# Kernel optimization log

Measured on AMD Instinct MI355X. Metric: run time of the kernel, lower is better.

The kernel has to match this reference:

```python
import jax, jax.numpy as jnp
import numpy as np

K_EXPERTS = 2  # init kwarg k_experts

def _glu_mlp(x, up_w, gate_w, down_w):
    # gated MLP: down( up(x) * GELU(gate(x)) ), exact-erf GELU matching torch nn.GELU()
    h = (x @ up_w) * jax.nn.gelu(x @ gate_w, approximate=False)
    return h @ down_w

def setup_inputs() -> dict:
    key = jax.random.key(0)
    ks = jax.random.split(key, 8)
    B, S, D, I, E = 2, 2048, 1024, 512, 8
    sc = 0.02
    return {
        "x": jax.random.normal(ks[0], (B, S, D), jnp.float32),
        "gate_w": jax.random.normal(ks[1], (E, D), jnp.float32) * sc,
        "up_w": jax.random.normal(ks[2], (E, D, I), jnp.float32) * sc,
        "gproj_w": jax.random.normal(ks[3], (E, D, I), jnp.float32) * sc,
        "down_w": jax.random.normal(ks[4], (E, I, D), jnp.float32) * sc,
        "shared_up_w": jax.random.normal(ks[5], (D, I), jnp.float32) * sc,
        "shared_gate_w": jax.random.normal(ks[6], (D, I), jnp.float32) * sc,
        "shared_down_w": jax.random.normal(ks[7], (I, D), jnp.float32) * sc,
    }

def reference(x, gate_w, up_w, gproj_w, down_w, shared_up_w, shared_gate_w, shared_down_w):
    B, S, D = x.shape
    E = gate_w.shape[0]
    xf = x.reshape(-1, D)                      # [T, D]
    T = xf.shape[0]

    # --- SigmaGate: softmax over expert logits, top-k, renormalize ---
    logits = xf @ gate_w.T                     # [T, E]
    scores = jax.nn.softmax(logits, axis=-1)
    topk_w, topk_idx = jax.lax.top_k(scores, K_EXPERTS)   # [T, k]
    topk_w = topk_w / (topk_w.sum(axis=-1, keepdims=True) + 1e-20)

    # combine weights as dense [T, E] (topk indices are distinct per token)
    combine = jnp.zeros((T, E), xf.dtype).at[jnp.arange(T)[:, None], topk_idx].add(topk_w)

    # --- experts: scan over E, accumulate weighted expert outputs ---
    def step(acc, ws):
        uw, gw, dw, ce = ws                    # ce: [T] combine weight for this expert
        y_e = _glu_mlp(xf, uw, gw, dw)         # [T, D]
        return acc + ce[:, None] * y_e, None

    y, _ = jax.lax.scan(step, jnp.zeros_like(xf), (up_w, gproj_w, down_w, combine.T))

    # --- shared expert on identity ---
    y = y + _glu_mlp(xf, shared_up_w, shared_gate_w, shared_down_w)
    return y.reshape(B, S, D)
```

## Files before the change

### kernel.cpp

```cpp
#include <hip/hip_runtime.h>
#include <hip/hip_bf16.h>
#include <math.h>

#define T_TOK 4096
#define D_DIM 1024
#define I_DIM 512
#define E_EXP 8
#define KSEL 2
#define NPAIR (T_TOK * KSEL)
#define ROUTED_CAP 10240
#define SHARED_BASE ROUTED_CAP
#define RTOT (ROUTED_CAP + T_TOK)
#define MAXTILES 56
#define GRID_G (MAXTILES * 4)
#define NTRB 3456

typedef __bf16 bf16x8 __attribute__((ext_vector_type(8)));
typedef float f32x4 __attribute__((ext_vector_type(4)));
typedef unsigned short ushort8 __attribute__((ext_vector_type(8)));

constexpr size_t SZ_XB  = (size_t)T_TOK * D_DIM * 2;
constexpr size_t SZ_UG  = (size_t)E_EXP * 2 * I_DIM * D_DIM * 2;
constexpr size_t SZ_DT  = (size_t)E_EXP * I_DIM * D_DIM * 2;
constexpr size_t SZ_SUG = (size_t)2 * I_DIM * D_DIM * 2;
constexpr size_t SZ_SDT = (size_t)I_DIM * D_DIM * 2;
constexpr size_t SZ_H   = (size_t)RTOT * I_DIM * 2;
constexpr size_t SZ_Y   = (size_t)RTOT * D_DIM * 2;

constexpr size_t OFF_XB   = 0;
constexpr size_t OFF_UG   = OFF_XB  + SZ_XB;
constexpr size_t OFF_DT   = OFF_UG  + SZ_UG;
constexpr size_t OFF_SUG  = OFF_DT  + SZ_DT;
constexpr size_t OFF_SDT  = OFF_SUG + SZ_SUG;
constexpr size_t OFF_H    = OFF_SDT + SZ_SDT;
constexpr size_t OFF_Y    = OFF_H   + SZ_H;
constexpr size_t OFF_TOPKI= OFF_Y   + SZ_Y;
constexpr size_t OFF_TOPKW= OFF_TOPKI + (size_t)NPAIR * 4;
constexpr size_t OFF_INV  = OFF_TOPKW + (size_t)NPAIR * 4;
constexpr size_t OFF_PERM = OFF_INV   + (size_t)NPAIR * 4;
constexpr size_t OFF_META = OFF_PERM  + (size_t)RTOT * 4;

__device__ __forceinline__ unsigned short f2bf(float f) {
  unsigned int u = __float_as_uint(f);
  unsigned int r = (u + 0x7FFFu + ((u >> 16) & 1u)) >> 16;
  return (unsigned short)r;
}
__device__ __forceinline__ float bf2f(unsigned short s) {
  return __uint_as_float(((unsigned int)s) << 16);
}
__device__ __forceinline__ void gload_lds16(const void* g, void* l) {
  __builtin_amdgcn_global_load_lds(
      (const __attribute__((address_space(1))) void*)g,
      (__attribute__((address_space(3))) void*)l, 16, 0, 0);
}

__global__ __launch_bounds__(256) void prep_kernel(
    const float* __restrict__ x,   const float* __restrict__ gw,
    const float* __restrict__ upw, const float* __restrict__ gpw,
    const float* __restrict__ dww, const float* __restrict__ sup,
    const float* __restrict__ sgt, const float* __restrict__ sdw,
    unsigned short* __restrict__ UG, unsigned short* __restrict__ sUG,
    unsigned short* __restrict__ Dt, unsigned short* __restrict__ sDt,
    unsigned short* __restrict__ xb,
    int* __restrict__ topk_idx, float* __restrict__ topk_w) {
  __shared__ float t[64][65];
  int bid = blockIdx.x, tid = threadIdx.x;
  if (bid < NTRB) {
    const float* in; unsigned short* out;
    int R, C, xt, yt, mode;
    if (bid < 1024)      { int e = bid >> 7, s = bid & 127;
      in = upw + (size_t)e * D_DIM * I_DIM; out = UG + (size_t)e * 2 * I_DIM * D_DIM;
      R = D_DIM; C = I_DIM; xt = s & 7; yt = s >> 3; mode = 0; }
    else if (bid < 2048) { int b = bid - 1024; int e = b >> 7, s = b & 127;
      in = gpw + (size_t)e * D_DIM * I_DIM; out = UG + (size_t)e * 2 * I_DIM * D_DIM;
      R = D_DIM; C = I_DIM; xt = s & 7; yt = s >> 3; mode = 1; }
    else if (bid < 3072) { int b = bid - 2048; int e = b >> 7, s = b & 127;
      in = dww + (size_t)e * I_DIM * D_DIM; out = Dt + (size_t)e * I_DIM * D_DIM;
      R = I_DIM; C = D_DIM; xt = s & 15; yt = s >> 4; mode = 2; }
    else if (bid < 3200) { int s = bid - 3072;
      in = sup; out = sUG; R = D_DIM; C = I_DIM; xt = s & 7; yt = s >> 3; mode = 0; }
    else if (bid < 3328) { int s = bid - 3200;
      in = sgt; out = sUG; R = D_DIM; C = I_DIM; xt = s & 7; yt = s >> 3; mode = 1; }
    else                 { int s = bid - 3328;
      in = sdw; out = sDt; R = I_DIM; C = D_DIM; xt = s & 15; yt = s >> 4; mode = 2; }
    int c0 = xt * 64, r0 = yt * 64;
    int tx = tid & 63, ty = tid >> 6;
#pragma unroll
    for (int i = 0; i < 16; ++i)
      t[ty + 4 * i][tx] = in[(size_t)(r0 + ty + 4 * i) * C + c0 + tx];
    __syncthreads();
#pragma unroll
    for (int i = 0; i < 16; ++i) {
      int c = c0 + ty + 4 * i;
      int orow = (mode == 2) ? c : (((c >> 4) << 5) + (c & 15) + (mode == 1 ? 16 : 0));
      out[(size_t)orow * R + r0 + tx] = f2bf(t[tx][ty + 4 * i]);
    }
  } else {
    int lane = tid & 63;
    int tok = (bid - NTRB) * 4 + (tid >> 6);
    const float4* xr = (const float4*)(x + (size_t)tok * D_DIM);
    float4 xv[4];
#pragma unroll
    for (int j = 0; j < 4; ++j) xv[j] = xr[lane + 64 * j];
#pragma unroll
    for (int j = 0; j < 4; ++j) {
      ushort4 o;
      o.x = f2bf(xv[j].x); o.y = f2bf(xv[j].y); o.z = f2bf(xv[j].z); o.w = f2bf(xv[j].w);
      *(ushort4*)&xb[(size_t)tok * D_DIM + (lane + 64 * j) * 4] = o;
    }
    float acc[E_EXP];
#pragma unroll
    for (int e = 0; e < E_EXP; ++e) {
      const float4* gr = (const float4*)(gw + (size_t)e * D_DIM);
      float a = 0.f;
#pragma unroll
      for (int j = 0; j < 4; ++j) {
        float4 g = gr[lane + 64 * j];
        a += xv[j].x * g.x + xv[j].y * g.y + xv[j].z * g.z + xv[j].w * g.w;
      }
      acc[e] = a;
    }
#pragma unroll
    for (int off = 32; off; off >>= 1)
#pragma unroll
      for (int e = 0; e < E_EXP; ++e) acc[e] += __shfl_xor(acc[e], off, 64);
    if (lane == 0) {
      int i0 = 0; float m0 = acc[0];
#pragma unroll
      for (int e = 1; e < E_EXP; ++e) if (acc[e] > m0) { m0 = acc[e]; i0 = e; }
      int i1 = -1; float m1 = -1e30f;
#pragma unroll
      for (int e = 0; e < E_EXP; ++e) if (e != i0 && acc[e] > m1) { m1 = acc[e]; i1 = e; }
      float e1 = __expf(m1 - m0);
      float w0 = 1.0f / (1.0f + e1);
      float w1 = e1 / (1.0f + e1);
      topk_idx[2 * tok] = i0; topk_idx[2 * tok + 1] = i1;
      topk_w[2 * tok] = w0;   topk_w[2 * tok + 1] = w1;
    }
  }
}

__global__ __launch_bounds__(1024) void route_kernel(
    const int* __restrict__ tidx, int* __restrict__ meta,
    int* __restrict__ perm, int* __restrict__ inv) {
  __shared__ int els[NPAIR];
  __shared__ int cnt_iw[128][E_EXP];
  __shared__ int base_iw[128][E_EXP];
  __shared__ int ebase[E_EXP];
  __shared__ int ecnt[E_EXP];
  int tid = threadIdx.x, lane = tid & 63, wv = tid >> 6;

  for (int it = 0; it < NPAIR / 1024; ++it) {
    int g = it * 1024 + tid;
    int e = tidx[g];
    els[g] = e;
#pragma unroll
    for (int ex = 0; ex < E_EXP; ++ex) {
      unsigned long long m = __ballot(e == ex);
      if (lane == 0) cnt_iw[it * 16 + wv][ex] = __popcll(m);
    }
  }
  __syncthreads();

  if (tid < E_EXP) {
    int s = 0;
    for (int iw = 0; iw < 128; ++iw) { base_iw[iw][tid] = s; s += cnt_iw[iw][tid]; }
    ecnt[tid] = s;
  }
  __syncthreads();

  if (tid == 0) {
    int o = 0, tc = 0;
    int2* m2 = (int2*)meta;
    for (int e = 0; e < E_EXP; ++e) {
      ebase[e] = o;
      int c = ecnt[e];
      int pt = (c + 255) >> 8;
      for (int ti = 0; ti < pt; ++ti) m2[tc++] = make_int2(e, o + ti * 256);
      o += pt * 256;
    }
    for (int ti = 0; ti < T_TOK / 256; ++ti)
      m2[tc++] = make_int2(E_EXP, SHARED_BASE + ti * 256);
    for (; tc < MAXTILES; ++tc) m2[tc] = make_int2(-1, 0);
  }
  __syncthreads();

  for (int it = 0; it < NPAIR / 1024; ++it) {
    int g = it * 1024 + tid;
    int e = els[g];
    int rank = 0;
#pragma unroll
    for (int ex = 0; ex < E_EXP; ++ex) {
      unsigned long long m = __ballot(e == ex);
      if (e == ex) rank = __popcll(m & ((1ull << lane) - 1ull));
    }
    int row = ebase[e] + base_iw[it * 16 + wv][e] + rank;
    perm[row] = g >> 1;
    inv[g] = row;
  }
  for (int p = tid; p < E_EXP * 256; p += 1024) {
    int e = p >> 8, s = p & 255;
    int c = ecnt[e];
    int padn = (((c + 255) >> 8) << 8) - c;
    if (s < padn) perm[ebase[e] + c + s] = 0;
  }
  for (int t = tid; t < T_TOK; t += 1024) perm[SHARED_BASE + t] = t;
}

__global__ __launch_bounds__(512, 2) void gemm1_kernel(
    const unsigned short* __restrict__ xb, const unsigned short* __restrict__ UG,
    const unsigned short* __restrict__ sUG, unsigned short* __restrict__ H,
    const int* __restrict__ meta, const int* __restrict__ perm) {
  int orig = blockIdx.x;
  int wg = (orig & 7) * (GRID_G / 8) + (orig >> 3);
  int mt = wg >> 2, nt = wg & 3;
  int2 m2 = ((const int2*)meta)[mt];
  int e = m2.x;
  if (e < 0) return;
  int base = m2.y;
  int n0 = nt * 256;
  const unsigned short* B = (e < E_EXP) ? UG + (size_t)e * 2 * I_DIM * D_DIM : sUG;

  __shared__ unsigned short As[2 * 256 * 64];
  __shared__ unsigned short Bs[2 * 256 * 64];

  int tid = threadIdx.x, lane = tid & 63, wv = tid >> 6;
  const unsigned short *gA[4], *gB[4];
  int dL[4];
#pragma unroll
  for (int j = 0; j < 4; ++j) {
    int c = j * 512 + tid;
    int row = c >> 3, q = c & 7, qs = q ^ (row & 7);
    int tok = perm[base + row];
    gA[j] = xb + (size_t)tok * D_DIM + qs * 8;
    gB[j] = B + (size_t)(n0 + row) * D_DIM + qs * 8;
    dL[j] = (j * 512 + wv * 64) * 8;
  }

  f32x4 acc[8][4] = {};
  int wr = (wv >> 2) * 128, wc = (wv & 3) * 64;
  int l15 = lane & 15, l4 = lane >> 4;
  int sx = l15 & 7;

#define STAGE1(buf, k0) do { \
  _Pragma("unroll") \
  for (int j = 0; j < 4; ++j) { \
    gload_lds16(gA[j] + (k0), As + (buf) * 16384 + dL[j]); \
    gload_lds16(gB[j] + (k0), Bs + (buf) * 16384 + dL[j]); \
  } } while (0)

  STAGE1(0, 0);
  const int NK = D_DIM / 64;
  for (int t = 0; t < NK; ++t) {
    int cur = t & 1;
    if (t + 1 < NK) {
      STAGE1(cur ^ 1, (t + 1) * 64);
      asm volatile("s_waitcnt vmcnt(8)" ::: "memory");
    } else {
      asm volatile("s_waitcnt vmcnt(0)" ::: "memory");
    }
    __builtin_amdgcn_s_barrier();
#pragma unroll
    for (int kh = 0; kh < 2; ++kh) {
      int kb = kh * 4 + l4;
      bf16x8 af[8], bfr[4];
#pragma unroll
      for (int i = 0; i < 8; ++i)
        af[i] = *reinterpret_cast<const bf16x8*>(&As[cur * 16384 + (wr + i * 16 + l15) * 64 + ((kb ^ sx)) * 8]);
#pragma unroll
      for (int j = 0; j < 4; ++j)
        bfr[j] = *reinterpret_cast<const bf16x8*>(&Bs[cur * 16384 + (wc + j * 16 + l15) * 64 + ((kb ^ sx)) * 8]);
      __builtin_amdgcn_s_setprio(1);
#pragma unroll
      for (int i = 0; i < 8; ++i)
#pragma unroll
        for (int j = 0; j < 4; ++j)
          acc[i][j] = __builtin_amdgcn_mfma_f32_16x16x32_bf16(af[i], bfr[j], acc[i][j], 0, 0, 0);
      __builtin_amdgcn_s_setprio(0);
    }
    asm volatile("s_waitcnt lgkmcnt(0)" ::: "memory");
    __builtin_amdgcn_s_barrier();
  }
#undef STAGE1

  const float is2 = 0.70710678118654752f;
  int cb = ((n0 + wc) >> 1);
#pragma unroll
  for (int i = 0; i < 8; ++i) {
    int row = base + wr + i * 16 + l4 * 4;
#pragma unroll
    for (int p = 0; p < 2; ++p) {
      int col = cb + p * 16 + l15;
#pragma unroll
      for (int r = 0; r < 4; ++r) {
        float u = acc[i][2 * p][r], g = acc[i][2 * p + 1][r];
        float gl = 0.5f * g * (1.0f + erff(g * is2));
        H[(size_t)(row + r) * I_DIM + col] = f2bf(u * gl);
      }
    }
  }
}

__global__ __launch_bounds__(512, 2) void gemm2_kernel(
    const unsigned short* __restrict__ H, const unsigned short* __restrict__ Dt,
    const unsigned short* __restrict__ sDt, unsigned short* __restrict__ Y,
    const int* __restrict__ meta) {
  int orig = blockIdx.x;
  int wg = (orig & 7) * (GRID_G / 8) + (orig >> 3);
  int mt = wg >> 2, nt = wg & 3;
  int2 m2 = ((const int2*)meta)[mt];
  int e = m2.x;
  if (e < 0) return;
  int base = m2.y;
  int n0 = nt * 256;
  const unsigned short* B = (e < E_EXP) ? Dt + (size_t)e * D_DIM * I_DIM : sDt;

  __shared__ unsigned short As[2 * 256 * 64];
  __shared__ unsigned short Bs[2 * 256 * 64];

  int tid = threadIdx.x, lane = tid & 63, wv = tid >> 6;
  const unsigned short *gA[4], *gB[4];
  int dL[4];
#pragma unroll
  for (int j = 0; j < 4; ++j) {
    int c = j * 512 + tid;
    int row = c >> 3, q = c & 7, qs = q ^ (row & 7);
    gA[j] = H + (size_t)(base + row) * I_DIM + qs * 8;
    gB[j] = B + (size_t)(n0 + row) * I_DIM + qs * 8;
    dL[j] = (j * 512 + wv * 64) * 8;
  }

  f32x4 acc[8][4] = {};
  int wr = (wv >> 2) * 128, wc = (wv & 3) * 64;
  int l15 = lane & 15, l4 = lane >> 4;
  int sx = l15 & 7;

#define STAGE2(buf, k0) do { \
  _Pragma("unroll") \
  for (int j = 0; j < 4; ++j) { \
    gload_lds16(gA[j] + (k0), As + (buf) * 16384 + dL[j]); \
    gload_lds16(gB[j] + (k0), Bs + (buf) * 16384 + dL[j]); \
  } } while (0)

  STAGE2(0, 0);
  const int NK = I_DIM / 64;
  for (int t = 0; t < NK; ++t) {
    int cur = t & 1;
    if (t + 1 < NK) {
      STAGE2(cur ^ 1, (t + 1) * 64);
      asm volatile("s_waitcnt vmcnt(8)" ::: "memory");
    } else {
      asm volatile("s_waitcnt vmcnt(0)" ::: "memory");
    }
    __builtin_amdgcn_s_barrier();
#pragma unroll
    for (int kh = 0; kh < 2; ++kh) {
      int kb = kh * 4 + l4;
      bf16x8 af[8], bfr[4];
#pragma unroll
      for (int i = 0; i < 8; ++i)
        af[i] = *reinterpret_cast<const bf16x8*>(&As[cur * 16384 + (wr + i * 16 + l15) * 64 + ((kb ^ sx)) * 8]);
#pragma unroll
      for (int j = 0; j < 4; ++j)
        bfr[j] = *reinterpret_cast<const bf16x8*>(&Bs[cur * 16384 + (wc + j * 16 + l15) * 64 + ((kb ^ sx)) * 8]);
      __builtin_amdgcn_s_setprio(1);
#pragma unroll
      for (int i = 0; i < 8; ++i)
#pragma unroll
        for (int j = 0; j < 4; ++j)
          acc[i][j] = __builtin_amdgcn_mfma_f32_16x16x32_bf16(af[i], bfr[j], acc[i][j], 0, 0, 0);
      __builtin_amdgcn_s_setprio(0);
    }
    asm volatile("s_waitcnt lgkmcnt(0)" ::: "memory");
    __builtin_amdgcn_s_barrier();
  }
#undef STAGE2

#pragma unroll
  for (int i = 0; i < 8; ++i) {
    int row = base + wr + i * 16 + l4 * 4;
#pragma unroll
    for (int j = 0; j < 4; ++j) {
      int col = n0 + wc + j * 16 + l15;
#pragma unroll
      for (int r = 0; r < 4; ++r)
        Y[(size_t)(row + r) * D_DIM + col] = f2bf(acc[i][j][r]);
    }
  }
}

__global__ void combine_kernel(const unsigned short* __restrict__ Y, const int* __restrict__ inv,
                               const float* __restrict__ tw, float* __restrict__ out) {
  int g = blockIdx.x * 256 + threadIdx.x;
  int t = g >> 7, d0 = (g & 127) * 8;
  int r0 = inv[2 * t], r1 = inv[2 * t + 1];
  float w0 = tw[2 * t], w1 = tw[2 * t + 1];
  ushort8 y0 = *(const ushort8*)&Y[(size_t)r0 * D_DIM + d0];
  ushort8 y1 = *(const ushort8*)&Y[(size_t)r1 * D_DIM + d0];
  ushort8 ys = *(const ushort8*)&Y[(size_t)(SHARED_BASE + t) * D_DIM + d0];
  float o[8];
#pragma unroll
  for (int j = 0; j < 8; ++j)
    o[j] = w0 * bf2f(y0[j]) + w1 * bf2f(y1[j]) + bf2f(ys[j]);
  float4* op = (float4*)(out + (size_t)t * D_DIM + d0);
  op[0] = make_float4(o[0], o[1], o[2], o[3]);
  op[1] = make_float4(o[4], o[5], o[6], o[7]);
}

extern "C" void kernel_launch(void* const* d_in, const int* in_sizes, int n_in,
                              void* d_out, int out_size, void* d_ws, size_t ws_size,
                              hipStream_t stream) {
  const float* x    = (const float*)d_in[0];
  const float* gw   = (const float*)d_in[1];
  const float* upw  = (const float*)d_in[2];
  const float* gpw  = (const float*)d_in[3];
  const float* dww  = (const float*)d_in[4];
  const float* sup  = (const float*)d_in[5];
  const float* sgt  = (const float*)d_in[6];
  const float* sdw  = (const float*)d_in[7];
  float* out = (float*)d_out;

  char* ws = (char*)d_ws;
  unsigned short* xb  = (unsigned short*)(ws + OFF_XB);
  unsigned short* UG  = (unsigned short*)(ws + OFF_UG);
  unsigned short* Dt  = (unsigned short*)(ws + OFF_DT);
  unsigned short* sUG = (unsigned short*)(ws + OFF_SUG);
  unsigned short* sDt = (unsigned short*)(ws + OFF_SDT);
  unsigned short* H   = (unsigned short*)(ws + OFF_H);
  unsigned short* Y   = (unsigned short*)(ws + OFF_Y);
  int*   tki   = (int*)(ws + OFF_TOPKI);
  float* tkw   = (float*)(ws + OFF_TOPKW);
  int*   inv   = (int*)(ws + OFF_INV);
  int*   perm  = (int*)(ws + OFF_PERM);
  int*   meta  = (int*)(ws + OFF_META);

  prep_kernel<<<NTRB + T_TOK / 4, 256, 0, stream>>>(x, gw, upw, gpw, dww, sup, sgt, sdw,
                                                    UG, sUG, Dt, sDt, xb, tki, tkw);
  route_kernel<<<1, 1024, 0, stream>>>(tki, meta, perm, inv);

  gemm1_kernel<<<GRID_G, 512, 0, stream>>>(xb, UG, sUG, H, meta, perm);
  gemm2_kernel<<<GRID_G, 512, 0, stream>>>(H, Dt, sDt, Y, meta);
  combine_kernel<<<(T_TOK * 128) / 256, 256, 0, stream>>>(Y, inv, tkw, out);
}
```

Measured before the change: 108.1 us.

## Fuse expert combine into down-projection epilogue via weighted atomic adds

```diff
diff --git a/kernel.cpp b/kernel.cpp
--- a/kernel.cpp
+++ b/kernel.cpp
@@ -14,6 +14,8 @@
 #define MAXTILES 56
 #define GRID_G (MAXTILES * 4)
 #define NTRB 3456
+#define NGATB (T_TOK / 4)
+#define NZB 1024
 
 typedef __bf16 bf16x8 __attribute__((ext_vector_type(8)));
 typedef float f32x4 __attribute__((ext_vector_type(4)));
@@ -25,7 +27,6 @@
 constexpr size_t SZ_SUG = (size_t)2 * I_DIM * D_DIM * 2;
 constexpr size_t SZ_SDT = (size_t)I_DIM * D_DIM * 2;
 constexpr size_t SZ_H   = (size_t)RTOT * I_DIM * 2;
-constexpr size_t SZ_Y   = (size_t)RTOT * D_DIM * 2;
 
 constexpr size_t OFF_XB   = 0;
 constexpr size_t OFF_UG   = OFF_XB  + SZ_XB;
@@ -33,20 +34,16 @@
 constexpr size_t OFF_SUG  = OFF_DT  + SZ_DT;
 constexpr size_t OFF_SDT  = OFF_SUG + SZ_SUG;
 constexpr size_t OFF_H    = OFF_SDT + SZ_SDT;
-constexpr size_t OFF_Y    = OFF_H   + SZ_H;
-constexpr size_t OFF_TOPKI= OFF_Y   + SZ_Y;
+constexpr size_t OFF_TOPKI= OFF_H   + SZ_H;
 constexpr size_t OFF_TOPKW= OFF_TOPKI + (size_t)NPAIR * 4;
-constexpr size_t OFF_INV  = OFF_TOPKW + (size_t)NPAIR * 4;
-constexpr size_t OFF_PERM = OFF_INV   + (size_t)NPAIR * 4;
+constexpr size_t OFF_WROW = OFF_TOPKW + (size_t)NPAIR * 4;
+constexpr size_t OFF_PERM = OFF_WROW  + (size_t)RTOT * 4;
 constexpr size_t OFF_META = OFF_PERM  + (size_t)RTOT * 4;
 
 __device__ __forceinline__ unsigned short f2bf(float f) {
   unsigned int u = __float_as_uint(f);
   unsigned int r = (u + 0x7FFFu + ((u >> 16) & 1u)) >> 16;
   return (unsigned short)r;
-}
-__device__ __forceinline__ float bf2f(unsigned short s) {
-  return __uint_as_float(((unsigned int)s) << 16);
 }
 __device__ __forceinline__ void gload_lds16(const void* g, void* l) {
   __builtin_amdgcn_global_load_lds(
@@ -62,27 +59,28 @@
     unsigned short* __restrict__ UG, unsigned short* __restrict__ sUG,
     unsigned short* __restrict__ Dt, unsigned short* __restrict__ sDt,
     unsigned short* __restrict__ xb,
-    int* __restrict__ topk_idx, float* __restrict__ topk_w) {
+    int* __restrict__ topk_idx, float* __restrict__ topk_w,
+    float* __restrict__ out) {
   __shared__ float t[64][65];
   int bid = blockIdx.x, tid = threadIdx.x;
   if (bid < NTRB) {
-    const float* in; unsigned short* out;
+    const float* in; unsigned short* outw;
     int R, C, xt, yt, mode;
     if (bid < 1024)      { int e = bid >> 7, s = bid & 127;
-      in = upw + (size_t)e * D_DIM * I_DIM; out = UG + (size_t)e * 2 * I_DIM * D_DIM;
+      in = upw + (size_t)e * D_DIM * I_DIM; outw = UG + (size_t)e * 2 * I_DIM * D_DIM;
       R = D_DIM; C = I_DIM; xt = s & 7; yt = s >> 3; mode = 0; }
     else if (bid < 2048) { int b = bid - 1024; int e = b >> 7, s = b & 127;
-      in = gpw + (size_t)e * D_DIM * I_DIM; out = UG + (size_t)e * 2 * I_DIM * D_DIM;
+      in = gpw + (size_t)e * D_DIM * I_DIM; outw = UG + (size_t)e * 2 * I_DIM * D_DIM;
       R = D_DIM; C = I_DIM; xt = s & 7; yt = s >> 3; mode = 1; }
     else if (bid < 3072) { int b = bid - 2048; int e = b >> 7, s = b & 127;
-      in = dww + (size_t)e * I_DIM * D_DIM; out = Dt + (size_t)e * I_DIM * D_DIM;
+      in = dww + (size_t)e * I_DIM * D_DIM; outw = Dt + (size_t)e * I_DIM * D_DIM;
       R = I_DIM; C = D_DIM; xt = s & 15; yt = s >> 4; mode = 2; }
     else if (bid < 3200) { int s = bid - 3072;
-      in = sup; out = sUG; R = D_DIM; C = I_DIM; xt = s & 7; yt = s >> 3; mode = 0; }
+      in = sup; outw = sUG; R = D_DIM; C = I_DIM; xt = s & 7; yt = s >> 3; mode = 0; }
     else if (bid < 3328) { int s = bid - 3200;
-      in = sgt; out = sUG; R = D_DIM; C = I_DIM; xt = s & 7; yt = s >> 3; mode = 1; }
+      in = sgt; outw = sUG; R = D_DIM; C = I_DIM; xt = s & 7; yt = s >> 3; mode = 1; }
     else                 { int s = bid - 3328;
-      in = sdw; out = sDt; R = I_DIM; C = D_DIM; xt = s & 15; yt = s >> 4; mode = 2; }
+      in = sdw; outw = sDt; R = I_DIM; C = D_DIM; xt = s & 15; yt = s >> 4; mode = 2; }
     int c0 = xt * 64, r0 = yt * 64;
     int tx = tid & 63, ty = tid >> 6;
 #pragma unroll
@@ -93,9 +91,9 @@
     for (int i = 0; i < 16; ++i) {
       int c = c0 + ty + 4 * i;
       int orow = (mode == 2) ? c : (((c >> 4) << 5) + (c & 15) + (mode == 1 ? 16 : 0));
-      out[(size_t)orow * R + r0 + tx] = f2bf(t[tx][ty + 4 * i]);
-    }
-  } else {
+      outw[(size_t)orow * R + r0 + tx] = f2bf(t[tx][ty + 4 * i]);
+    }
+  } else if (bid < NTRB + NGATB) {
     int lane = tid & 63;
     int tok = (bid - NTRB) * 4 + (tid >> 6);
     const float4* xr = (const float4*)(x + (size_t)tok * D_DIM);
@@ -137,12 +135,19 @@
       topk_idx[2 * tok] = i0; topk_idx[2 * tok + 1] = i1;
       topk_w[2 * tok] = w0;   topk_w[2 * tok + 1] = w1;
     }
+  } else {
+    int zb = bid - (NTRB + NGATB);
+    float4* o4 = (float4*)out;
+    float4 z = make_float4(0.f, 0.f, 0.f, 0.f);
+#pragma unroll
+    for (int it = 0; it < 4; ++it)
+      o4[(size_t)zb * 1024 + it * 256 + tid] = z;
   }
 }
 
 __global__ __launch_bounds__(1024) void route_kernel(
-    const int* __restrict__ tidx, int* __restrict__ meta,
-    int* __restrict__ perm, int* __restrict__ inv) {
+    const int* __restrict__ tidx, const float* __restrict__ tkw,
+    int* __restrict__ meta, int* __restrict__ perm, float* __restrict__ wrow) {
   __shared__ int els[NPAIR];
   __shared__ int cnt_iw[128][E_EXP];
   __shared__ int base_iw[128][E_EXP];
@@ -196,15 +201,17 @@
     }
     int row = ebase[e] + base_iw[it * 16 + wv][e] + rank;
     perm[row] = g >> 1;
-    inv[g] = row;
+    wrow[row] = tkw[g];
   }
   for (int p = tid; p < E_EXP * 256; p += 1024) {
     int e = p >> 8, s = p & 255;
     int c = ecnt[e];
     int padn = (((c + 255) >> 8) << 8) - c;
-    if (s < padn) perm[ebase[e] + c + s] = 0;
-  }
-  for (int t = tid; t < T_TOK; t += 1024) perm[SHARED_BASE + t] = t;
+    if (s < padn) { perm[ebase[e] + c + s] = 0; wrow[ebase[e] + c + s] = 0.f; }
+  }
+  for (int t = tid; t < T_TOK; t += 1024) {
+    perm[SHARED_BASE + t] = t; wrow[SHARED_BASE + t] = 1.f;
+  }
 }
 
 __global__ __launch_bounds__(512, 2) void gemm1_kernel(
@@ -303,8 +310,9 @@
 
 __global__ __launch_bounds__(512, 2) void gemm2_kernel(
     const unsigned short* __restrict__ H, const unsigned short* __restrict__ Dt,
-    const unsigned short* __restrict__ sDt, unsigned short* __restrict__ Y,
-    const int* __restrict__ meta) {
+    const unsigned short* __restrict__ sDt, float* __restrict__ out,
+    const int* __restrict__ meta, const int* __restrict__ perm,
+    const float* __restrict__ wrow) {
   int orig = blockIdx.x;
   int wg = (orig & 7) * (GRID_G / 8) + (orig >> 3);
   int mt = wg >> 2, nt = wg & 3;
@@ -378,33 +386,20 @@
 
 #pragma unroll
   for (int i = 0; i < 8; ++i) {
-    int row = base + wr + i * 16 + l4 * 4;
+    int lrow = base + wr + i * 16 + l4 * 4;
+    int toks[4]; float wv4[4];
+#pragma unroll
+    for (int r = 0; r < 4; ++r) { toks[r] = perm[lrow + r]; wv4[r] = wrow[lrow + r]; }
 #pragma unroll
     for (int j = 0; j < 4; ++j) {
       int col = n0 + wc + j * 16 + l15;
 #pragma unroll
-      for (int r = 0; r < 4; ++r)
-        Y[(size_t)(row + r) * D_DIM + col] = f2bf(acc[i][j][r]);
-    }
-  }
-}
-
-__global__ void combine_kernel(const unsigned short* __restrict__ Y, const int* __restrict__ inv,
-                               const float* __restrict__ tw, float* __restrict__ out) {
-  int g = blockIdx.x * 256 + threadIdx.x;
-  int t = g >> 7, d0 = (g & 127) * 8;
-  int r0 = inv[2 * t], r1 = inv[2 * t + 1];
-  float w0 = tw[2 * t], w1 = tw[2 * t + 1];
-  ushort8 y0 = *(const ushort8*)&Y[(size_t)r0 * D_DIM + d0];
-  ushort8 y1 = *(const ushort8*)&Y[(size_t)r1 * D_DIM + d0];
-  ushort8 ys = *(const ushort8*)&Y[(size_t)(SHARED_BASE + t) * D_DIM + d0];
-  float o[8];
-#pragma unroll
-  for (int j = 0; j < 8; ++j)
-    o[j] = w0 * bf2f(y0[j]) + w1 * bf2f(y1[j]) + bf2f(ys[j]);
-  float4* op = (float4*)(out + (size_t)t * D_DIM + d0);
-  op[0] = make_float4(o[0], o[1], o[2], o[3]);
-  op[1] = make_float4(o[4], o[5], o[6], o[7]);
+      for (int r = 0; r < 4; ++r) {
+        if (wv4[r] != 0.0f)
+          atomicAdd(&out[(size_t)toks[r] * D_DIM + col], wv4[r] * acc[i][j][r]);
+      }
+    }
+  }
 }
 
 extern "C" void kernel_launch(void* const* d_in, const int* in_sizes, int n_in,
@@ -427,18 +422,16 @@
   unsigned short* sUG = (unsigned short*)(ws + OFF_SUG);
   unsigned short* sDt = (unsigned short*)(ws + OFF_SDT);
   unsigned short* H   = (unsigned short*)(ws + OFF_H);
-  unsigned short* Y   = (unsigned short*)(ws + OFF_Y);
   int*   tki   = (int*)(ws + OFF_TOPKI);
   float* tkw   = (float*)(ws + OFF_TOPKW);
-  int*   inv   = (int*)(ws + OFF_INV);
+  float* wrow  = (float*)(ws + OFF_WROW);
   int*   perm  = (int*)(ws + OFF_PERM);
   int*   meta  = (int*)(ws + OFF_META);
 
-  prep_kernel<<<NTRB + T_TOK / 4, 256, 0, stream>>>(x, gw, upw, gpw, dww, sup, sgt, sdw,
-                                                    UG, sUG, Dt, sDt, xb, tki, tkw);
-  route_kernel<<<1, 1024, 0, stream>>>(tki, meta, perm, inv);
+  prep_kernel<<<NTRB + NGATB + NZB, 256, 0, stream>>>(x, gw, upw, gpw, dww, sup, sgt, sdw,
+                                                      UG, sUG, Dt, sDt, xb, tki, tkw, out);
+  route_kernel<<<1, 1024, 0, stream>>>(tki, tkw, meta, perm, wrow);
 
   gemm1_kernel<<<GRID_G, 512, 0, stream>>>(xb, UG, sUG, H, meta, perm);
-  gemm2_kernel<<<GRID_G, 512, 0, stream>>>(H, Dt, sDt, Y, meta);
-  combine_kernel<<<(T_TOK * 128) / 256, 256, 0, stream>>>(Y, inv, tkw, out);
-}
+  gemm2_kernel<<<GRID_G, 512, 0, stream>>>(H, Dt, sDt, out, meta, perm, wrow);
+}
```

Result: slower. 134.4 us (+24.4%).
